# Kernel tuning notes

Hardware: AMD Instinct MI355X
Metric: run time of the kernel (lower is better)

The kernel has to match this reference:

```python
import jax, jax.numpy as jnp
import numpy as np

D_MODEL = 1024
N_HEADS = 16
HEAD_DIM = D_MODEL // N_HEADS
D_FF = 4096
SEQ = 2048
BATCH = 4
THETA = 10000.0
EPS = 1e-5


def rmsnorm(x, w, eps=EPS):
    xf = x.astype(jnp.float32)
    var = jnp.mean(xf * xf, axis=-1, keepdims=True) + eps
    return (xf * jax.lax.rsqrt(var) * w).astype(x.dtype)


def rope_tables(head_dim, max_len, theta):
    freqs = 1.0 / theta ** (jnp.arange(0, head_dim, 2, dtype=jnp.float32) / head_dim)
    t = jnp.arange(max_len, dtype=jnp.float32)
    ang = jnp.outer(t, freqs)  # [T, Hs/2]
    return jnp.cos(ang), jnp.sin(ang)


def apply_rope(x, cos, sin):
    # x: [B, H, T, Hs]; cos/sin: [T, Hs/2] (broadcast over B, H)
    x1 = x[..., 0::2]
    x2 = x[..., 1::2]
    o1 = x1 * cos - x2 * sin
    o2 = x1 * sin + x2 * cos
    return jnp.stack([o1, o2], axis=-1).reshape(x.shape).astype(x.dtype)


def setup_inputs() -> dict:
    key = jax.random.key(0)
    ks = jax.random.split(key, 12)
    s = 0.02
    return {
        "x": jax.random.normal(ks[0], (BATCH, SEQ, D_MODEL), dtype=jnp.float32),
        "token_positions": jnp.arange(SEQ, dtype=jnp.int32),
        "ln1_w": jnp.ones((D_MODEL,), dtype=jnp.float32),
        "q_w": jax.random.normal(ks[1], (D_MODEL, D_MODEL), dtype=jnp.float32) * s,
        "k_w": jax.random.normal(ks[2], (D_MODEL, D_MODEL), dtype=jnp.float32) * s,
        "v_w": jax.random.normal(ks[3], (D_MODEL, D_MODEL), dtype=jnp.float32) * s,
        "o_w": jax.random.normal(ks[4], (D_MODEL, D_MODEL), dtype=jnp.float32) * s,
        "ln2_w": jnp.ones((D_MODEL,), dtype=jnp.float32),
        "w1": jax.random.normal(ks[5], (D_FF, D_MODEL), dtype=jnp.float32) * s,
        "w2": jax.random.normal(ks[6], (D_MODEL, D_FF), dtype=jnp.float32) * s,
        "w3": jax.random.normal(ks[7], (D_FF, D_MODEL), dtype=jnp.float32) * s,
    }


def reference(x, token_positions, ln1_w, q_w, k_w, v_w, o_w, ln2_w, w1, w2, w3):
    B, T, D = x.shape
    cos_full, sin_full = rope_tables(HEAD_DIM, SEQ, THETA)
    cos = cos_full[token_positions]
    sin = sin_full[token_positions]

    # --- attention sublayer ---
    h = rmsnorm(x, ln1_w)
    q = jnp.einsum('btd,od->bto', h, q_w)
    k = jnp.einsum('btd,od->bto', h, k_w)
    v = jnp.einsum('btd,od->bto', h, v_w)
    # [B, T, D] -> [B, H, T, Hs]
    def split_heads(t_):
        return t_.reshape(B, T, N_HEADS, HEAD_DIM).transpose(0, 2, 1, 3)
    xq, xk, xv = split_heads(q), split_heads(k), split_heads(v)
    xq = apply_rope(xq, cos, sin)
    xk = apply_rope(xk, cos, sin)

    scores = jnp.einsum('bhqd,bhkd->bhqk', xq, xk) / jnp.sqrt(jnp.float32(HEAD_DIM))
    causal = jnp.tril(jnp.ones((T, T), dtype=bool))
    scores = jnp.where(causal, scores, jnp.float32(-jnp.inf))
    attn = jax.nn.softmax(scores, axis=-1)
    ctx = jnp.einsum('bhqk,bhkd->bhqd', attn, xv)
    ctx = ctx.transpose(0, 2, 1, 3).reshape(B, T, D)
    x = x + jnp.einsum('btd,od->bto', ctx, o_w)

    # --- SwiGLU FFN sublayer ---
    h2 = rmsnorm(x, ln2_w)
    a = jnp.einsum('btd,fd->btf', h2, w1)
    g = jnp.einsum('btd,fd->btf', h2, w3)
    ff = jnp.einsum('btf,df->btd', a * jax.nn.sigmoid(a) * g, w2)
    return x + ff
```

## Files before the change

kernel.cpp:

```cpp
#include <hip/hip_runtime.h>
#include <hip/hip_bf16.h>

#define D_MODEL 1024
#define N_HEADS 16
#define HEAD_DIM 64
#define D_FF 4096
#define SEQ 2048
#define BATCH 4
#define NTOK (BATCH*SEQ)
#define QS 3072

typedef __attribute__((ext_vector_type(4))) float  f32x4;
typedef __attribute__((ext_vector_type(8))) short  s16x8;
typedef __attribute__((ext_vector_type(4))) unsigned short u16x4;

typedef __attribute__((address_space(1))) const unsigned int gas_u32;
typedef __attribute__((address_space(3))) unsigned int las_u32;

__device__ __forceinline__ void gload_lds16(const void* g, void* l) {
  __builtin_amdgcn_global_load_lds((gas_u32*)g, (las_u32*)l, 16, 0, 0);
}

__device__ __forceinline__ float bf2f(unsigned short u) {
  union { unsigned int i; float f; } v; v.i = ((unsigned int)u) << 16; return v.f;
}
__device__ __forceinline__ unsigned short f2bf(float f) {
  union { float f; unsigned int i; } v; v.f = f;
  return (unsigned short)((v.i + 0x7fffu + ((v.i >> 16) & 1u)) >> 16);
}

__global__ __launch_bounds__(256) void cvt_k(const float* __restrict__ in,
                                             unsigned short* __restrict__ out, int n) {
  for (long i = ((long)blockIdx.x*256 + threadIdx.x)*4; i < n; i += (long)gridDim.x*1024) {
    f32x4 v = *(const f32x4*)&in[i];
    u16x4 o;
    #pragma unroll
    for (int c=0;c<4;c++) o[c] = f2bf(v[c]);
    *(u16x4*)&out[i] = o;
  }
}

__global__ __launch_bounds__(256) void rope_tables_k(const int* __restrict__ pos,
                                                     float* __restrict__ cosT,
                                                     float* __restrict__ sinT) {
  int idx = blockIdx.x*256 + threadIdx.x;
  int t = idx >> 5, i = idx & 31;
  float p  = (float)pos[t];
  float fr = powf(10000.0f, -(float)i * (1.0f/32.0f));
  float ang = p * fr;
  cosT[idx] = cosf(ang);
  sinT[idx] = sinf(ang);
}

__global__ __launch_bounds__(256) void rmsnorm_k(const float* __restrict__ x,
                                                 const float* __restrict__ wgt,
                                                 unsigned short* __restrict__ out) {
  const long row = blockIdx.x;
  const int t = threadIdx.x;
  f32x4 v = *(const f32x4*)&x[row*D_MODEL + t*4];
  float ss = v[0]*v[0] + v[1]*v[1] + v[2]*v[2] + v[3]*v[3];
  #pragma unroll
  for (int off=1; off<64; off<<=1) ss += __shfl_xor(ss, off, 64);
  __shared__ float red[4];
  if ((t & 63) == 0) red[t >> 6] = ss;
  __syncthreads();
  float tot = red[0] + red[1] + red[2] + red[3];
  float inv = rsqrtf(tot * (1.0f/D_MODEL) + 1e-5f);
  f32x4 wv = *(const f32x4*)&wgt[t*4];
  u16x4 o;
  #pragma unroll
  for (int c=0;c<4;c++) o[c] = f2bf(v[c] * inv * wv[c]);
  *(u16x4*)&out[row*D_MODEL + t*4] = o;
}

__global__ __launch_bounds__(256) void rope_k(unsigned short* __restrict__ qkv,
                                              const float* __restrict__ cosT,
                                              const float* __restrict__ sinT) {
  long idx = (long)blockIdx.x*256 + threadIdx.x;
  int ig = (int)(idx & 7);
  long th = idx >> 3;
  int h = (int)(th & 15);
  long bt = th >> 4;
  int t = (int)(bt & (SEQ-1));
  long off = bt*QS + h*HEAD_DIM + ig*8;
  f32x4 cs = *(const f32x4*)&cosT[t*32 + ig*4];
  f32x4 sn = *(const f32x4*)&sinT[t*32 + ig*4];
  s16x8 qv = *(const s16x8*)&qkv[off];
  s16x8 kv = *(const s16x8*)&qkv[off + 1024];
  s16x8 qo, ko;
  #pragma unroll
  for (int p=0;p<4;p++) {
    float q1 = bf2f((unsigned short)qv[2*p]), q2 = bf2f((unsigned short)qv[2*p+1]);
    qo[2*p]   = (short)f2bf((q1*cs[p] - q2*sn[p]) * 0.125f);
    qo[2*p+1] = (short)f2bf((q1*sn[p] + q2*cs[p]) * 0.125f);
    float k1 = bf2f((unsigned short)kv[2*p]), k2 = bf2f((unsigned short)kv[2*p+1]);
    ko[2*p]   = (short)f2bf(k1*cs[p] - k2*sn[p]);
    ko[2*p+1] = (short)f2bf(k1*sn[p] + k2*cs[p]);
  }
  *(s16x8*)&qkv[off] = qo;
  *(s16x8*)&qkv[off + 1024] = ko;
}

template<int EPI>
__global__ __launch_bounds__(256) void gemm_bt(const unsigned short* __restrict__ A,
                                               const unsigned short* __restrict__ W,
                                               unsigned short* __restrict__ Cb,
                                               float* __restrict__ Cf,
                                               const float* __restrict__ resid,
                                               int M, int N, int K) {
  __shared__ __align__(16) unsigned short As[128*64];
  __shared__ __align__(16) unsigned short Bs[128*64];

  const int nwg = gridDim.x * gridDim.y;
  int orig = blockIdx.y * gridDim.x + blockIdx.x;
  int swz = orig;
  if ((nwg & 7) == 0) {
    int cpx = nwg >> 3;
    swz = (orig & 7) * cpx + (orig >> 3);
  }
  const int bx = swz % gridDim.x;
  const int by = swz / gridDim.x;

  const int tid = threadIdx.x;
  const int w  = tid >> 6;
  const int l  = tid & 63;
  const int lr = l & 15;
  const int lg = l >> 4;
  const int wm = (w >> 1) * 64;
  const int wn = (w & 1) * 64;

  const long rowA0 = (long)by * 128;
  const long rowB0 = (long)bx * 128;

  f32x4 acc[4][4] = {};

  for (int kt = 0; kt < K; kt += 64) {
    #pragma unroll
    for (int it = 0; it < 4; ++it) {
      int chunk = it*256 + tid;
      int row = chunk >> 3;
      int csw = (chunk & 7) ^ (row & 7);
      gload_lds16(&A[(rowA0 + row)*(long)K + kt + csw*8], &As[chunk*8]);
    }
    #pragma unroll
    for (int it = 0; it < 4; ++it) {
      int chunk = it*256 + tid;
      int row = chunk >> 3;
      int csw = (chunk & 7) ^ (row & 7);
      gload_lds16(&W[(rowB0 + row)*(long)K + kt + csw*8], &Bs[chunk*8]);
    }
    __syncthreads();

    s16x8 af[2][4], bfv[2][4];
    #pragma unroll
    for (int m=0;m<4;m++) {
      int row = wm + m*16 + lr;
      #pragma unroll
      for (int kk=0;kk<2;kk++) {
        int sw = (kk*4+lg) ^ (row & 7);
        af[kk][m] = *(const s16x8*)&As[row*64 + sw*8];
      }
    }
    #pragma unroll
    for (int n=0;n<4;n++) {
      int row = wn + n*16 + lr;
      #pragma unroll
      for (int kk=0;kk<2;kk++) {
        int sw = (kk*4+lg) ^ (row & 7);
        bfv[kk][n] = *(const s16x8*)&Bs[row*64 + sw*8];
      }
    }
    #pragma unroll
    for (int kk=0;kk<2;kk++)
      #pragma unroll
      for (int m=0;m<4;m++)
        #pragma unroll
        for (int n=0;n<4;n++)
          acc[m][n] = __builtin_amdgcn_mfma_f32_16x16x32_bf16(af[kk][m], bfv[kk][n], acc[m][n], 0,0,0);
    __syncthreads();
  }

  #pragma unroll
  for (int m=0;m<4;m++)
    #pragma unroll
    for (int n=0;n<4;n++)
      #pragma unroll
      for (int r=0;r<4;r++) {
        long row = rowA0 + wm + m*16 + lg*4 + r;
        long col = rowB0 + wn + n*16 + lr;
        float val = acc[m][n][r];
        if constexpr (EPI == 0) {
          Cb[row*(long)N + col] = f2bf(val);
        } else {
          Cf[row*(long)N + col] = resid[row*(long)N + col] + val;
        }
      }
}

template<int EPI>
__global__ __launch_bounds__(256) void gemm_db(const unsigned short* __restrict__ A,
                                               const unsigned short* __restrict__ W,
                                               unsigned short* __restrict__ Cb,
                                               float* __restrict__ Cf,
                                               const float* __restrict__ resid,
                                               int M, int N, int K) {
  __shared__ __align__(16) unsigned short As[2][128*64];
  __shared__ __align__(16) unsigned short Bs[2][128*64];

  const int nwg = gridDim.x * gridDim.y;
  int orig = blockIdx.y * gridDim.x + blockIdx.x;
  int swz = orig;
  if ((nwg & 7) == 0) {
    int cpx = nwg >> 3;
    swz = (orig & 7) * cpx + (orig >> 3);
  }
  const int bx = swz % gridDim.x;
  const int by = swz / gridDim.x;

  const int tid = threadIdx.x;
  const int w  = tid >> 6;
  const int l  = tid & 63;
  const int lr = l & 15;
  const int lg = l >> 4;
  const int wm = (w >> 1) * 64;
  const int wn = (w & 1) * 64;

  const long rowA0 = (long)by * 128;
  const long rowB0 = (long)bx * 128;

  f32x4 acc[4][4] = {};
  const int nk = K >> 6;

  #pragma unroll
  for (int it = 0; it < 4; ++it) {
    int chunk = it*256 + tid;
    int row = chunk >> 3;
    int csw = (chunk & 7) ^ (row & 7);
    gload_lds16(&A[(rowA0 + row)*(long)K + csw*8], &As[0][chunk*8]);
    gload_lds16(&W[(rowB0 + row)*(long)K + csw*8], &Bs[0][chunk*8]);
  }
  __syncthreads();

  int cur = 0;
  for (int ki = 0; ki < nk; ++ki) {
    if (ki + 1 < nk) {
      int kt = (ki + 1) << 6;
      #pragma unroll
      for (int it = 0; it < 4; ++it) {
        int chunk = it*256 + tid;
        int row = chunk >> 3;
        int csw = (chunk & 7) ^ (row & 7);
        gload_lds16(&A[(rowA0 + row)*(long)K + kt + csw*8], &As[cur^1][chunk*8]);
        gload_lds16(&W[(rowB0 + row)*(long)K + kt + csw*8], &Bs[cur^1][chunk*8]);
      }
    }
    s16x8 af[2][4], bfv[2][4];
    #pragma unroll
    for (int m=0;m<4;m++) {
      int row = wm + m*16 + lr;
      #pragma unroll
      for (int kk=0;kk<2;kk++) {
        int sw = (kk*4+lg) ^ (row & 7);
        af[kk][m] = *(const s16x8*)&As[cur][row*64 + sw*8];
      }
    }
    #pragma unroll
    for (int n=0;n<4;n++) {
      int row = wn + n*16 + lr;
      #pragma unroll
      for (int kk=0;kk<2;kk++) {
        int sw = (kk*4+lg) ^ (row & 7);
        bfv[kk][n] = *(const s16x8*)&Bs[cur][row*64 + sw*8];
      }
    }
    #pragma unroll
    for (int kk=0;kk<2;kk++)
      #pragma unroll
      for (int m=0;m<4;m++)
        #pragma unroll
        for (int n=0;n<4;n++)
          acc[m][n] = __builtin_amdgcn_mfma_f32_16x16x32_bf16(af[kk][m], bfv[kk][n], acc[m][n], 0,0,0);
    __syncthreads();
    cur ^= 1;
  }

  #pragma unroll
  for (int m=0;m<4;m++)
    #pragma unroll
    for (int n=0;n<4;n++)
      #pragma unroll
      for (int r=0;r<4;r++) {
        long row = rowA0 + wm + m*16 + lg*4 + r;
        long col = rowB0 + wn + n*16 + lr;
        float val = acc[m][n][r];
        if constexpr (EPI == 0) {
          Cb[row*(long)N + col] = f2bf(val);
        } else {
          Cf[row*(long)N + col] = resid[row*(long)N + col] + val;
        }
      }
}

__global__ __launch_bounds__(256) void attn_k(const unsigned short* __restrict__ QKV,
                                              unsigned short* __restrict__ O) {
  const int bh = blockIdx.x;
  const int b = bh >> 4;
  const int h = bh & 15;
  const int tid = threadIdx.x;
  const int w  = tid >> 6;
  const int l  = tid & 63;
  const int lr = l & 15;
  const int lg = l >> 4;

  const unsigned short* Qp = QKV;
  const unsigned short* Kp = QKV + 1024;
  const unsigned short* Vp = QKV + 2048;

  __shared__ __align__(16) unsigned short Ks[2][64*64];
  __shared__ __align__(16) unsigned short Vs[2][64*64];
  __shared__ __align__(16) unsigned short Ps[4][16][64];

  const int skv = tid >> 2;
  const int sd0 = (tid & 3) * 16;
  const long hbase = (long)(b*SEQ)*QS + h*HEAD_DIM;

  for (int pass = 0; pass < 2; ++pass) {
    const int qt = pass ? 31 - (int)blockIdx.y : (int)blockIdx.y;
    const int q0 = qt * 64;
    const int ntile = qt + 1;

    const long rowQ = (long)(b*SEQ + q0 + w*16 + lr);
    s16x8 qf0 = *(const s16x8*)&Qp[rowQ*QS + h*HEAD_DIM + lg*8];
    s16x8 qf1 = *(const s16x8*)&Qp[rowQ*QS + h*HEAD_DIM + 32 + lg*8];

    float mi = -1e30f, li = 0.f;
    f32x4 oa[4] = {};

    #pragma unroll
    for (int it=0; it<2; ++it) {
      int chunk = it*256 + tid;
      int row = chunk >> 3;
      int csw = (chunk & 7) ^ (row & 7);
      gload_lds16(&Kp[hbase + (long)row*QS + csw*8], &Ks[0][chunk*8]);
    }
    {
      const unsigned short* src = &Vp[hbase + (long)skv*QS + sd0];
      s16x8 v0 = *(const s16x8*)&src[0];
      s16x8 v1 = *(const s16x8*)&src[8];
      #pragma unroll
      for (int i=0;i<16;i++) {
        int d = sd0 + i;
        int key = (d&7) ^ ((d>>3)&7);
        int c = (skv>>3) ^ key;
        Vs[0][d*64 + c*8 + (skv&7)] = (unsigned short)(i<8 ? v0[i] : v1[i-8]);
      }
    }
    __syncthreads();

    for (int t=0; t<ntile; ++t) {
      const int kv0 = t*64;
      const int cur = t & 1;
      const int nb  = cur ^ 1;
      const bool more = (t+1 < ntile);

      s16x8 v0, v1;
      if (more) {
        #pragma unroll
        for (int it=0; it<2; ++it) {
          int chunk = it*256 + tid;
          int row = chunk >> 3;
          int csw = (chunk & 7) ^ (row & 7);
          gload_lds16(&Kp[hbase + (long)(kv0 + 64 + row)*QS + csw*8], &Ks[nb][chunk*8]);
        }
        const unsigned short* src = &Vp[hbase + (long)(kv0 + 64 + skv)*QS + sd0];
        v0 = *(const s16x8*)&src[0];
        v1 = *(const s16x8*)&src[8];
      }

      f32x4 s[4];
      __builtin_amdgcn_s_setprio(1);
      #pragma unroll
      for (int j=0;j<4;j++) {
        int krow = j*16 + lr;
        s16x8 kf0 = *(const s16x8*)&Ks[cur][krow*64 + ((lg)     ^ (krow&7))*8];
        s16x8 kf1 = *(const s16x8*)&Ks[cur][krow*64 + ((4 + lg) ^ (krow&7))*8];
        f32x4 acc = {};
        acc = __builtin_amdgcn_mfma_f32_16x16x32_bf16(kf0, qf0, acc, 0,0,0);
        acc = __builtin_amdgcn_mfma_f32_16x16x32_bf16(kf1, qf1, acc, 0,0,0);
        s[j] = acc;
      }
      __builtin_amdgcn_s_setprio(0);

      if (t == ntile-1) {
        #pragma unroll
        for (int j=0;j<4;j++)
          #pragma unroll
          for (int r=0;r<4;r++)
            if (kv0 + j*16 + lg*4 + r > q0 + w*16 + lr) s[j][r] = -1e30f;
      }

      float pmax = s[0][0];
      #pragma unroll
      for (int j=0;j<4;j++)
        #pragma unroll
        for (int r=0;r<4;r++) pmax = fmaxf(pmax, s[j][r]);
      pmax = fmaxf(pmax, __shfl_xor(pmax, 16, 64));
      pmax = fmaxf(pmax, __shfl_xor(pmax, 32, 64));
      float mn = fmaxf(mi, pmax);
      float al = __expf(mi - mn);
      mi = mn;
      float psum = 0.f;
      #pragma unroll
      for (int j=0;j<4;j++)
        #pragma unroll
        for (int r=0;r<4;r++) {
          float p = __expf(s[j][r] - mn);
          s[j][r] = p;
          psum += p;
        }
      psum += __shfl_xor(psum, 16, 64);
      psum += __shfl_xor(psum, 32, 64);
      li = li*al + psum;

      float alq[4];
      #pragma unroll
      for (int r=0;r<4;r++) alq[r] = __shfl(al, lg*4 + r, 64);
      #pragma unroll
      for (int d=0;d<4;d++)
        #pragma unroll
        for (int r=0;r<4;r++) oa[d][r] *= alq[r];

      #pragma unroll
      for (int j=0;j<4;j++)
        #pragma unroll
        for (int r=0;r<4;r++) {
          int k = j*16 + lg*4 + r;
          int pos = ((k>>3) ^ (lr&7))*8 + (k&7);
          Ps[w][lr][pos] = f2bf(s[j][r]);
        }

      if (more) {
        #pragma unroll
        for (int i=0;i<16;i++) {
          int d = sd0 + i;
          int key = (d&7) ^ ((d>>3)&7);
          int c = (skv>>3) ^ key;
          Vs[nb][d*64 + c*8 + (skv&7)] = (unsigned short)(i<8 ? v0[i] : v1[i-8]);
        }
      }

      __builtin_amdgcn_s_setprio(1);
      #pragma unroll
      for (int kk=0;kk<2;kk++) {
        s16x8 pa = *(const s16x8*)&Ps[w][lr][((kk*4 + lg) ^ (lr&7))*8];
        #pragma unroll
        for (int d=0;d<4;d++) {
          int vrow = d*16 + lr;
          int key = (vrow&7) ^ ((vrow>>3)&7);
          int c = (kk*4 + lg) ^ key;
          s16x8 vb = *(const s16x8*)&Vs[cur][vrow*64 + c*8];
          oa[d] = __builtin_amdgcn_mfma_f32_16x16x32_bf16(pa, vb, oa[d], 0,0,0);
        }
      }
      __builtin_amdgcn_s_setprio(0);
      __syncthreads();
    }

    float liq[4];
    #pragma unroll
    for (int r=0;r<4;r++) liq[r] = __shfl(li, lg*4 + r, 64);
    #pragma unroll
    for (int d=0;d<4;d++)
      #pragma unroll
      for (int r=0;r<4;r++) {
        long row = (long)(b*SEQ + q0 + w*16 + lg*4 + r);
        O[row*D_MODEL + h*HEAD_DIM + d*16 + lr] = f2bf(oa[d][r] / liq[r]);
      }
  }
}

__global__ __launch_bounds__(256) void swiglu_k(unsigned short* __restrict__ a,
                                                const unsigned short* __restrict__ g) {
  long i = ((long)blockIdx.x*256 + threadIdx.x)*8;
  s16x8 av = *(const s16x8*)&a[i];
  s16x8 gv = *(const s16x8*)&g[i];
  s16x8 o;
  #pragma unroll
  for (int c=0;c<8;c++) {
    float xx = bf2f((unsigned short)av[c]);
    float yy = bf2f((unsigned short)gv[c]);
    float sg = 1.0f / (1.0f + __expf(-xx));
    o[c] = (short)f2bf(xx * sg * yy);
  }
  *(s16x8*)&a[i] = o;
}

extern "C" void kernel_launch(void* const* d_in, const int* in_sizes, int n_in,
                              void* d_out, int out_size, void* d_ws, size_t ws_size,
                              hipStream_t stream) {
  (void)in_sizes; (void)n_in; (void)out_size; (void)ws_size;
  const float* x    = (const float*)d_in[0];
  const int*   tpos = (const int*)d_in[1];
  const float* ln1  = (const float*)d_in[2];
  const float* qw   = (const float*)d_in[3];
  const float* kw   = (const float*)d_in[4];
  const float* vw   = (const float*)d_in[5];
  const float* ow   = (const float*)d_in[6];
  const float* ln2  = (const float*)d_in[7];
  const float* w1   = (const float*)d_in[8];
  const float* w2   = (const float*)d_in[9];
  const float* w3   = (const float*)d_in[10];
  float* out = (float*)d_out;

  char* ws = (char*)d_ws;
  size_t off = 0;
  auto nalloc = [&](size_t b) { void* p = ws + off; off += (b + 255) & ~(size_t)255; return p; };

  unsigned short* wqkvb = (unsigned short*)nalloc((size_t)3072*D_MODEL*2);
  unsigned short* wob   = (unsigned short*)nalloc((size_t)D_MODEL*D_MODEL*2);
  unsigned short* w1b   = (unsigned short*)nalloc((size_t)D_FF*D_MODEL*2);
  unsigned short* w3b   = (unsigned short*)nalloc((size_t)D_FF*D_MODEL*2);
  unsigned short* w2b   = (unsigned short*)nalloc((size_t)D_MODEL*D_FF*2);
  float* cosT = (float*)nalloc((size_t)SEQ*32*4);
  float* sinT = (float*)nalloc((size_t)SEQ*32*4);
  unsigned short* hbuf = (unsigned short*)nalloc((size_t)NTOK*D_MODEL*2);
  unsigned short* qkv  = (unsigned short*)nalloc((size_t)NTOK*QS*2);
  unsigned short* ctxb = (unsigned short*)nalloc((size_t)NTOK*D_MODEL*2);
  float* x2 = (float*)nalloc((size_t)NTOK*D_MODEL*4);
  unsigned short* gbuf = (unsigned short*)nalloc((size_t)NTOK*D_FF*2);
  unsigned short* abuf = qkv;

  cvt_k<<<1024,256,0,stream>>>(qw, wqkvb,                 D_MODEL*D_MODEL);
  cvt_k<<<1024,256,0,stream>>>(kw, wqkvb + 1024*D_MODEL,  D_MODEL*D_MODEL);
  cvt_k<<<1024,256,0,stream>>>(vw, wqkvb + 2048*D_MODEL,  D_MODEL*D_MODEL);
  cvt_k<<<1024,256,0,stream>>>(ow, wob, D_MODEL*D_MODEL);
  cvt_k<<<2048,256,0,stream>>>(w1, w1b, D_FF*D_MODEL);
  cvt_k<<<2048,256,0,stream>>>(w2, w2b, D_MODEL*D_FF);
  cvt_k<<<2048,256,0,stream>>>(w3, w3b, D_FF*D_MODEL);
  rope_tables_k<<<SEQ*32/256,256,0,stream>>>(tpos, cosT, sinT);

  rmsnorm_k<<<NTOK,256,0,stream>>>(x, ln1, hbuf);
  gemm_bt<0><<<dim3(24,64),256,0,stream>>>(hbuf, wqkvb, qkv, nullptr, nullptr, NTOK, QS, D_MODEL);
  rope_k<<<4096,256,0,stream>>>(qkv, cosT, sinT);
  attn_k<<<dim3(64,16),256,0,stream>>>(qkv, ctxb);
  gemm_bt<1><<<dim3(8,64),256,0,stream>>>(ctxb, wob, nullptr, x2, x, NTOK, D_MODEL, D_MODEL);

  rmsnorm_k<<<NTOK,256,0,stream>>>(x2, ln2, hbuf);
  gemm_db<0><<<dim3(32,64),256,0,stream>>>(hbuf, w1b, abuf, nullptr, nullptr, NTOK, D_FF, D_MODEL);
  gemm_bt<0><<<dim3(32,64),256,0,stream>>>(hbuf, w3b, gbuf, nullptr, nullptr, NTOK, D_FF, D_MODEL);
  swiglu_k<<<(long)NTOK*D_FF/8/256,256,0,stream>>>(abuf, gbuf);
  gemm_bt<1><<<dim3(8,64),256,0,stream>>>(abuf, w2b, nullptr, out, x2, NTOK, D_MODEL, D_FF);
}
```

Baseline: 647.1 us.

## Replace GEMMs with 8-wave triple-buffered 256x128 tile kernel; fuse weight casts

Swaps the single- and double-buffered 128x128 GEMMs for one kernel with 512 threads, 256x128 output tiles and a three-stage LDS ring. Each k-step is split into two halves, with prefetch of the next-next tile interleaved between them, manual vmcnt waits and raised MFMA priority. The seven weight-conversion launches are merged into one kernel that dispatches on element range. This aims to hide global-load latency and cut launch overhead, at the cost of more LDS (about 144KB per block) and tighter barrier/waitcnt correctness.

```diff
diff --git a/kernel.cpp b/kernel.cpp
--- a/kernel.cpp
+++ b/kernel.cpp
@@ -29,15 +29,28 @@
   return (unsigned short)((v.i + 0x7fffu + ((v.i >> 16) & 1u)) >> 16);
 }
 
-__global__ __launch_bounds__(256) void cvt_k(const float* __restrict__ in,
-                                             unsigned short* __restrict__ out, int n) {
-  for (long i = ((long)blockIdx.x*256 + threadIdx.x)*4; i < n; i += (long)gridDim.x*1024) {
-    f32x4 v = *(const f32x4*)&in[i];
-    u16x4 o;
-    #pragma unroll
-    for (int c=0;c<4;c++) o[c] = f2bf(v[c]);
-    *(u16x4*)&out[i] = o;
-  }
+__global__ __launch_bounds__(256) void cvt_all_k(const float* __restrict__ qw, const float* __restrict__ kw,
+                                                 const float* __restrict__ vw, const float* __restrict__ ow,
+                                                 const float* __restrict__ w1, const float* __restrict__ w2,
+                                                 const float* __restrict__ w3,
+                                                 unsigned short* __restrict__ wqkv, unsigned short* __restrict__ wo,
+                                                 unsigned short* __restrict__ b1, unsigned short* __restrict__ b2,
+                                                 unsigned short* __restrict__ b3) {
+  const long MM = 1 << 20;
+  long e = ((long)blockIdx.x*256 + threadIdx.x)*4;
+  const float* src; unsigned short* dst; long off;
+  if      (e <    MM) { src = qw; dst = wqkv;        off = e; }
+  else if (e <  2*MM) { src = kw; dst = wqkv + MM;   off = e - MM; }
+  else if (e <  3*MM) { src = vw; dst = wqkv + 2*MM; off = e - 2*MM; }
+  else if (e <  4*MM) { src = ow; dst = wo;          off = e - 3*MM; }
+  else if (e <  8*MM) { src = w1; dst = b1;          off = e - 4*MM; }
+  else if (e < 12*MM) { src = w2; dst = b2;          off = e - 8*MM; }
+  else                { src = w3; dst = b3;          off = e - 12*MM; }
+  f32x4 v = *(const f32x4*)&src[off];
+  u16x4 o;
+  #pragma unroll
+  for (int c=0;c<4;c++) o[c] = f2bf(v[c]);
+  *(u16x4*)&dst[off] = o;
 }
 
 __global__ __launch_bounds__(256) void rope_tables_k(const int* __restrict__ pos,
@@ -102,197 +115,122 @@
 }
 
 template<int EPI>
-__global__ __launch_bounds__(256) void gemm_bt(const unsigned short* __restrict__ A,
-                                               const unsigned short* __restrict__ W,
-                                               unsigned short* __restrict__ Cb,
-                                               float* __restrict__ Cf,
-                                               const float* __restrict__ resid,
-                                               int M, int N, int K) {
-  __shared__ __align__(16) unsigned short As[128*64];
-  __shared__ __align__(16) unsigned short Bs[128*64];
+__global__ __launch_bounds__(512, 2) void gemm8p(const unsigned short* __restrict__ A,
+                                                 const unsigned short* __restrict__ W,
+                                                 unsigned short* __restrict__ Cb,
+                                                 float* __restrict__ Cf,
+                                                 const float* __restrict__ resid,
+                                                 int M, int N, int K) {
+  __shared__ __align__(16) unsigned short As[3][256*64];
+  __shared__ __align__(16) unsigned short Bs[3][128*64];
 
   const int nwg = gridDim.x * gridDim.y;
   int orig = blockIdx.y * gridDim.x + blockIdx.x;
   int swz = orig;
-  if ((nwg & 7) == 0) {
-    int cpx = nwg >> 3;
-    swz = (orig & 7) * cpx + (orig >> 3);
-  }
+  if ((nwg & 7) == 0) { int cpx = nwg >> 3; swz = (orig & 7) * cpx + (orig >> 3); }
   const int bx = swz % gridDim.x;
   const int by = swz / gridDim.x;
 
   const int tid = threadIdx.x;
-  const int w  = tid >> 6;
+  const int wid = tid >> 6;
   const int l  = tid & 63;
   const int lr = l & 15;
   const int lg = l >> 4;
-  const int wm = (w >> 1) * 64;
-  const int wn = (w & 1) * 64;
-
-  const long rowA0 = (long)by * 128;
+  const int wm = (wid >> 2) * 128;
+  const int wn = (wid & 3) * 32;
+
+  const long rowA0 = (long)by * 256;
   const long rowB0 = (long)bx * 128;
-
-  f32x4 acc[4][4] = {};
-
-  for (int kt = 0; kt < K; kt += 64) {
-    #pragma unroll
-    for (int it = 0; it < 4; ++it) {
-      int chunk = it*256 + tid;
-      int row = chunk >> 3;
-      int csw = (chunk & 7) ^ (row & 7);
-      gload_lds16(&A[(rowA0 + row)*(long)K + kt + csw*8], &As[chunk*8]);
-    }
-    #pragma unroll
-    for (int it = 0; it < 4; ++it) {
-      int chunk = it*256 + tid;
-      int row = chunk >> 3;
-      int csw = (chunk & 7) ^ (row & 7);
-      gload_lds16(&W[(rowB0 + row)*(long)K + kt + csw*8], &Bs[chunk*8]);
-    }
-    __syncthreads();
-
-    s16x8 af[2][4], bfv[2][4];
-    #pragma unroll
-    for (int m=0;m<4;m++) {
-      int row = wm + m*16 + lr;
-      #pragma unroll
-      for (int kk=0;kk<2;kk++) {
-        int sw = (kk*4+lg) ^ (row & 7);
-        af[kk][m] = *(const s16x8*)&As[row*64 + sw*8];
-      }
-    }
-    #pragma unroll
-    for (int n=0;n<4;n++) {
-      int row = wn + n*16 + lr;
-      #pragma unroll
-      for (int kk=0;kk<2;kk++) {
-        int sw = (kk*4+lg) ^ (row & 7);
-        bfv[kk][n] = *(const s16x8*)&Bs[row*64 + sw*8];
-      }
-    }
-    #pragma unroll
-    for (int kk=0;kk<2;kk++)
-      #pragma unroll
-      for (int m=0;m<4;m++)
-        #pragma unroll
-        for (int n=0;n<4;n++)
-          acc[m][n] = __builtin_amdgcn_mfma_f32_16x16x32_bf16(af[kk][m], bfv[kk][n], acc[m][n], 0,0,0);
-    __syncthreads();
-  }
-
-  #pragma unroll
-  for (int m=0;m<4;m++)
-    #pragma unroll
-    for (int n=0;n<4;n++)
-      #pragma unroll
-      for (int r=0;r<4;r++) {
-        long row = rowA0 + wm + m*16 + lg*4 + r;
-        long col = rowB0 + wn + n*16 + lr;
-        float val = acc[m][n][r];
-        if constexpr (EPI == 0) {
-          Cb[row*(long)N + col] = f2bf(val);
-        } else {
-          Cf[row*(long)N + col] = resid[row*(long)N + col] + val;
-        }
-      }
-}
-
-template<int EPI>
-__global__ __launch_bounds__(256) void gemm_db(const unsigned short* __restrict__ A,
-                                               const unsigned short* __restrict__ W,
-                                               unsigned short* __restrict__ Cb,
-                                               float* __restrict__ Cf,
-                                               const float* __restrict__ resid,
-                                               int M, int N, int K) {
-  __shared__ __align__(16) unsigned short As[2][128*64];
-  __shared__ __align__(16) unsigned short Bs[2][128*64];
-
-  const int nwg = gridDim.x * gridDim.y;
-  int orig = blockIdx.y * gridDim.x + blockIdx.x;
-  int swz = orig;
-  if ((nwg & 7) == 0) {
-    int cpx = nwg >> 3;
-    swz = (orig & 7) * cpx + (orig >> 3);
-  }
-  const int bx = swz % gridDim.x;
-  const int by = swz / gridDim.x;
-
-  const int tid = threadIdx.x;
-  const int w  = tid >> 6;
-  const int l  = tid & 63;
-  const int lr = l & 15;
-  const int lg = l >> 4;
-  const int wm = (w >> 1) * 64;
-  const int wn = (w & 1) * 64;
-
-  const long rowA0 = (long)by * 128;
-  const long rowB0 = (long)bx * 128;
-
-  f32x4 acc[4][4] = {};
   const int nk = K >> 6;
 
-  #pragma unroll
-  for (int it = 0; it < 4; ++it) {
-    int chunk = it*256 + tid;
+  auto stA = [&](int bf, int kt, int it) {
+    int chunk = it*512 + tid;
     int row = chunk >> 3;
     int csw = (chunk & 7) ^ (row & 7);
-    gload_lds16(&A[(rowA0 + row)*(long)K + csw*8], &As[0][chunk*8]);
-    gload_lds16(&W[(rowB0 + row)*(long)K + csw*8], &Bs[0][chunk*8]);
+    gload_lds16(&A[(rowA0 + row)*(long)K + kt + csw*8], &As[bf][chunk*8]);
+  };
+  auto stB = [&](int bf, int kt, int it) {
+    int chunk = it*512 + tid;
+    int row = chunk >> 3;
+    int csw = (chunk & 7) ^ (row & 7);
+    gload_lds16(&W[(rowB0 + row)*(long)K + kt + csw*8], &Bs[bf][chunk*8]);
+  };
+
+  f32x4 acc[8][2] = {};
+
+  stA(0,0,0); stA(0,0,1); stA(0,0,2); stA(0,0,3); stB(0,0,0); stB(0,0,1);
+  stA(1,64,0); stA(1,64,1); stA(1,64,2); stA(1,64,3); stB(1,64,0); stB(1,64,1);
+  asm volatile("s_waitcnt vmcnt(6)" ::: "memory");
+  __builtin_amdgcn_s_barrier();
+
+  int buf = 0;
+  for (int ki = 0; ki < nk; ++ki) {
+    const int sb = (buf >= 1) ? buf - 1 : buf + 2;
+    const int kt2 = (ki + 2) << 6;
+    const bool st = (ki + 2) < nk;
+
+    s16x8 af[2][4], bfr[2][2];
+    #pragma unroll
+    for (int m=0;m<4;m++) {
+      int r = wm + m*16 + lr;
+      #pragma unroll
+      for (int kk=0;kk<2;kk++)
+        af[kk][m] = *(const s16x8*)&As[buf][r*64 + ((kk*4+lg)^(r&7))*8];
+    }
+    #pragma unroll
+    for (int n=0;n<2;n++) {
+      int r = wn + n*16 + lr;
+      #pragma unroll
+      for (int kk=0;kk<2;kk++)
+        bfr[kk][n] = *(const s16x8*)&Bs[buf][r*64 + ((kk*4+lg)^(r&7))*8];
+    }
+    if (st) { stA(sb,kt2,0); stA(sb,kt2,1); stB(sb,kt2,0); }
+    __builtin_amdgcn_s_barrier();
+    __builtin_amdgcn_s_setprio(1);
+    #pragma unroll
+    for (int kk=0;kk<2;kk++)
+      #pragma unroll
+      for (int m=0;m<4;m++)
+        #pragma unroll
+        for (int n=0;n<2;n++)
+          acc[m][n] = __builtin_amdgcn_mfma_f32_16x16x32_bf16(af[kk][m], bfr[kk][n], acc[m][n], 0,0,0);
+    __builtin_amdgcn_s_setprio(0);
+    __builtin_amdgcn_s_barrier();
+
+    #pragma unroll
+    for (int m=0;m<4;m++) {
+      int r = wm + 64 + m*16 + lr;
+      #pragma unroll
+      for (int kk=0;kk<2;kk++)
+        af[kk][m] = *(const s16x8*)&As[buf][r*64 + ((kk*4+lg)^(r&7))*8];
+    }
+    if (st) { stA(sb,kt2,2); stA(sb,kt2,3); stB(sb,kt2,1); }
+    __builtin_amdgcn_s_barrier();
+    __builtin_amdgcn_s_setprio(1);
+    #pragma unroll
+    for (int kk=0;kk<2;kk++)
+      #pragma unroll
+      for (int m=0;m<4;m++)
+        #pragma unroll
+        for (int n=0;n<2;n++)
+          acc[4+m][n] = __builtin_amdgcn_mfma_f32_16x16x32_bf16(af[kk][m], bfr[kk][n], acc[4+m][n], 0,0,0);
+    __builtin_amdgcn_s_setprio(0);
+    if (st)             { asm volatile("s_waitcnt vmcnt(6)" ::: "memory"); }
+    else if (ki+1 < nk) { asm volatile("s_waitcnt vmcnt(0)" ::: "memory"); }
+    __builtin_amdgcn_s_barrier();
+
+    buf = (buf == 2) ? 0 : buf + 1;
   }
-  __syncthreads();
-
-  int cur = 0;
-  for (int ki = 0; ki < nk; ++ki) {
-    if (ki + 1 < nk) {
-      int kt = (ki + 1) << 6;
-      #pragma unroll
-      for (int it = 0; it < 4; ++it) {
-        int chunk = it*256 + tid;
-        int row = chunk >> 3;
-        int csw = (chunk & 7) ^ (row & 7);
-        gload_lds16(&A[(rowA0 + row)*(long)K + kt + csw*8], &As[cur^1][chunk*8]);
-        gload_lds16(&W[(rowB0 + row)*(long)K + kt + csw*8], &Bs[cur^1][chunk*8]);
-      }
-    }
-    s16x8 af[2][4], bfv[2][4];
-    #pragma unroll
-    for (int m=0;m<4;m++) {
-      int row = wm + m*16 + lr;
-      #pragma unroll
-      for (int kk=0;kk<2;kk++) {
-        int sw = (kk*4+lg) ^ (row & 7);
-        af[kk][m] = *(const s16x8*)&As[cur][row*64 + sw*8];
-      }
-    }
-    #pragma unroll
-    for (int n=0;n<4;n++) {
-      int row = wn + n*16 + lr;
-      #pragma unroll
-      for (int kk=0;kk<2;kk++) {
-        int sw = (kk*4+lg) ^ (row & 7);
-        bfv[kk][n] = *(const s16x8*)&Bs[cur][row*64 + sw*8];
-      }
-    }
-    #pragma unroll
-    for (int kk=0;kk<2;kk++)
-      #pragma unroll
-      for (int m=0;m<4;m++)
-        #pragma unroll
-        for (int n=0;n<4;n++)
-          acc[m][n] = __builtin_amdgcn_mfma_f32_16x16x32_bf16(af[kk][m], bfv[kk][n], acc[m][n], 0,0,0);
-    __syncthreads();
-    cur ^= 1;
-  }
-
-  #pragma unroll
-  for (int m=0;m<4;m++)
-    #pragma unroll
-    for (int n=0;n<4;n++)
-      #pragma unroll
-      for (int r=0;r<4;r++) {
-        long row = rowA0 + wm + m*16 + lg*4 + r;
+
+  #pragma unroll
+  for (int mi=0;mi<8;mi++)
+    #pragma unroll
+    for (int n=0;n<2;n++)
+      #pragma unroll
+      for (int rr=0;rr<4;rr++) {
+        long row = rowA0 + wm + mi*16 + lg*4 + rr;
         long col = rowB0 + wn + n*16 + lr;
-        float val = acc[m][n][r];
+        float val = acc[mi][n][rr];
         if constexpr (EPI == 0) {
           Cb[row*(long)N + col] = f2bf(val);
         } else {
@@ -530,24 +468,19 @@
   unsigned short* gbuf = (unsigned short*)nalloc((size_t)NTOK*D_FF*2);
   unsigned short* abuf = qkv;
 
-  cvt_k<<<1024,256,0,stream>>>(qw, wqkvb,                 D_MODEL*D_MODEL);
-  cvt_k<<<1024,256,0,stream>>>(kw, wqkvb + 1024*D_MODEL,  D_MODEL*D_MODEL);
-  cvt_k<<<1024,256,0,stream>>>(vw, wqkvb + 2048*D_MODEL,  D_MODEL*D_MODEL);
-  cvt_k<<<1024,256,0,stream>>>(ow, wob, D_MODEL*D_MODEL);
-  cvt_k<<<2048,256,0,stream>>>(w1, w1b, D_FF*D_MODEL);
-  cvt_k<<<2048,256,0,stream>>>(w2, w2b, D_MODEL*D_FF);
-  cvt_k<<<2048,256,0,stream>>>(w3, w3b, D_FF*D_MODEL);
+  cvt_all_k<<<16384,256,0,stream>>>(qw, kw, vw, ow, w1, w2, w3,
+                                    wqkvb, wob, w1b, w2b, w3b);
   rope_tables_k<<<SEQ*32/256,256,0,stream>>>(tpos, cosT, sinT);
 
   rmsnorm_k<<<NTOK,256,0,stream>>>(x, ln1, hbuf);
-  gemm_bt<0><<<dim3(24,64),256,0,stream>>>(hbuf, wqkvb, qkv, nullptr, nullptr, NTOK, QS, D_MODEL);
+  gemm8p<0><<<dim3(24,32),512,0,stream>>>(hbuf, wqkvb, qkv, nullptr, nullptr, NTOK, QS, D_MODEL);
   rope_k<<<4096,256,0,stream>>>(qkv, cosT, sinT);
   attn_k<<<dim3(64,16),256,0,stream>>>(qkv, ctxb);
-  gemm_bt<1><<<dim3(8,64),256,0,stream>>>(ctxb, wob, nullptr, x2, x, NTOK, D_MODEL, D_MODEL);
+  gemm8p<1><<<dim3(8,32),512,0,stream>>>(ctxb, wob, nullptr, x2, x, NTOK, D_MODEL, D_MODEL);
 
   rmsnorm_k<<<NTOK,256,0,stream>>>(x2, ln2, hbuf);
-  gemm_db<0><<<dim3(32,64),256,0,stream>>>(hbuf, w1b, abuf, nullptr, nullptr, NTOK, D_FF, D_MODEL);
-  gemm_bt<0><<<dim3(32,64),256,0,stream>>>(hbuf, w3b, gbuf, nullptr, nullptr, NTOK, D_FF, D_MODEL);
+  gemm8p<0><<<dim3(32,32),512,0,stream>>>(hbuf, w1b, abuf, nullptr, nullptr, NTOK, D_FF, D_MODEL);
+  gemm8p<0><<<dim3(32,32),512,0,stream>>>(hbuf, w3b, gbuf, nullptr, nullptr, NTOK, D_FF, D_MODEL);
   swiglu_k<<<(long)NTOK*D_FF/8/256,256,0,stream>>>(abuf, gbuf);
-  gemm_bt<1><<<dim3(8,64),256,0,stream>>>(abuf, w2b, nullptr, out, x2, NTOK, D_MODEL, D_FF);
-}
+  gemm8p<1><<<dim3(8,32),512,0,stream>>>(abuf, w2b, nullptr, out, x2, NTOK, D_MODEL, D_FF);
+}
```

New measurement: 637.8 us. No clear change (-1.4%).
